# Kernel tuning notes

Measured on AMD Instinct MI355X. Metric: run time of the kernel, lower is better.

## Reference

```python
import jax, jax.numpy as jnp
import numpy as np

BN_EPS = 1e-5
NUM_BITS = 8          # activation quantization bits
NUM_BITS_WEIGHT = 8   # weight quantization bits


def _ste(x, q):
    # straight-through estimator: forward = q, backward = identity
    return x + jax.lax.stop_gradient(q - x)


def quant_signed(x, bits):
    # symmetric signed per-tensor uniform quantization (input_signed=True / weights with sign=True)
    qmax = float(2 ** (bits - 1) - 1)
    scale = jnp.max(jnp.abs(x)) / qmax + 1e-12
    q = jnp.clip(jnp.round(x / scale), -qmax - 1.0, qmax) * scale
    return _ste(x, q)


def quant_unsigned(x, bits):
    # unsigned per-tensor uniform quantization (input_signed=False, post-ReLU activations)
    qmax = float(2 ** bits - 1)
    scale = jnp.max(x) / qmax + 1e-12
    q = jnp.clip(jnp.round(x / scale), 0.0, qmax) * scale
    return _ste(x, q)


def conv3x3(x, w, stride=1):
    # x: [N,C,H,W], w: [O,I,3,3], padding=1, no bias
    return jax.lax.conv_general_dilated(
        x, w, window_strides=(stride, stride), padding=((1, 1), (1, 1)),
        dimension_numbers=('NCHW', 'OIHW', 'NCHW'))


def batchnorm(x, gamma, beta):
    # training-mode BN: per-batch statistics over (N,H,W)
    mean = jnp.mean(x, axis=(0, 2, 3), keepdims=True)
    var = jnp.var(x, axis=(0, 2, 3), keepdims=True)
    xn = (x - mean) * jax.lax.rsqrt(var + BN_EPS)
    return xn * gamma[None, :, None, None] + beta[None, :, None, None]


def setup_inputs() -> dict:
    key = jax.random.key(0)
    k1, k2, k3 = jax.random.split(key, 3)
    B, C, H, W = 64, 256, 32, 32
    x = jax.random.normal(k1, (B, C, H, W), dtype=jnp.float32)
    fan = C * 9
    w1 = jax.random.normal(k2, (C, C, 3, 3), dtype=jnp.float32) * np.sqrt(2.0 / fan)
    w2 = jax.random.normal(k3, (C, C, 3, 3), dtype=jnp.float32) * np.sqrt(2.0 / fan)
    gamma1 = jnp.ones((C,), jnp.float32)
    beta1 = jnp.zeros((C,), jnp.float32)
    gamma2 = jnp.ones((C,), jnp.float32)
    beta2 = jnp.zeros((C,), jnp.float32)
    return {'x': x, 'w1': w1, 'gamma1': gamma1, 'beta1': beta1,
            'w2': w2, 'gamma2': gamma2, 'beta2': beta2}


def reference(x, w1, gamma1, beta1, w2, gamma2, beta2):
    residual = x
    # conv1: input_signed=True -> signed 8-bit act quant; weight 8-bit signed quant
    qx = quant_signed(x, NUM_BITS)
    qw1 = quant_signed(w1, NUM_BITS_WEIGHT)
    out = conv3x3(qx, qw1, stride=1)
    out = batchnorm(out, gamma1, beta1)
    out = jax.nn.relu(out)
    # conv2: input_signed=False -> unsigned 8-bit act quant (post-ReLU)
    qo = quant_unsigned(out, NUM_BITS)
    qw2 = quant_signed(w2, NUM_BITS_WEIGHT)
    out = conv3x3(qo, qw2, stride=1)
    out = batchnorm(out, gamma2, beta2)
    out = out + residual
    out = jax.nn.relu(out)
    return out
```

## Files before the change

### kernel.cpp

```cpp
#include <hip/hip_runtime.h>

typedef __attribute__((ext_vector_type(4))) int i32x4;
typedef __attribute__((ext_vector_type(4))) float f32x4;

typedef __attribute__((address_space(1))) unsigned int uglobal;
typedef __attribute__((address_space(3))) unsigned int ulocal;

__device__ __forceinline__ void async16(const void* g, void* l) {
  __builtin_amdgcn_global_load_lds((const uglobal*)g, (ulocal*)l, 16, 0, 0);
}
__device__ __forceinline__ float u2f(unsigned u) { return __uint_as_float(u); }

__global__ __launch_bounds__(256) void absmax3_kernel(const float* __restrict__ x,
                                                      const float* __restrict__ w1,
                                                      const float* __restrict__ w2,
                                                      unsigned* __restrict__ sc) {
  int b = blockIdx.x;
  const float* src; int n4, b0, nb, seg;
  if (b < 1792)      { src = x;  n4 = 4194304; b0 = 0;    nb = 1792; seg = 0; }
  else if (b < 1856) { src = w1; n4 = 147456;  b0 = 1792; nb = 64;   seg = 1; }
  else               { src = w2; n4 = 147456;  b0 = 1856; nb = 64;   seg = 2; }
  float m = 0.f;
  int stride = nb * 256;
  for (int i = (b - b0) * 256 + threadIdx.x; i < n4; i += stride) {
    float4 v = ((const float4*)src)[i];
    m = fmaxf(fmaxf(fabsf(v.x), fabsf(v.y)), fmaxf(fmaxf(fabsf(v.z), fabsf(v.w)), m));
  }
  for (int off = 32; off; off >>= 1) m = fmaxf(m, __shfl_down(m, off, 64));
  __shared__ float sm[4];
  int lane = threadIdx.x & 63, wv = threadIdx.x >> 6;
  if (!lane) sm[wv] = m;
  __syncthreads();
  if (threadIdx.x == 0)
    atomicMax(sc + seg, __float_as_uint(fmaxf(fmaxf(sm[0], sm[1]), fmaxf(sm[2], sm[3]))));
}

__global__ __launch_bounds__(256) void quantw_kernel(const float* __restrict__ w1,
                                                     const float* __restrict__ w2,
                                                     signed char* __restrict__ wq1,
                                                     signed char* __restrict__ wq2,
                                                     const unsigned* __restrict__ sc) {
  int b = blockIdx.x;
  int t2 = b >= 2304;
  const float* w = t2 ? w2 : w1;
  signed char* wq = t2 ? wq2 : wq1;
  float s = u2f(sc[1 + t2]) / 127.f + 1e-12f;
  int j = (b - t2 * 2304) * 256 + threadIdx.x;
  int o = j / 2304, k = j - o * 2304, tap = k >> 8, c = k & 255;
  float q = fminf(fmaxf(rintf(w[(size_t)(o * 256 + c) * 9 + tap] / s), -128.f), 127.f);
  wq[j] = (signed char)q;
}

__global__ __launch_bounds__(64) void tapsum_kernel(const signed char* __restrict__ wq2,
                                                    int* __restrict__ csumT) {
  int o = blockIdx.x;
  const int* row = (const int*)(wq2 + (size_t)o * 2304);
  int s = 0;
  for (int i = threadIdx.x; i < 576; i += 64) {
    int v = row[i];
    s += (int)(signed char)(v) + (int)(signed char)(v >> 8) +
         (int)(signed char)(v >> 16) + (int)(signed char)(v >> 24);
  }
  for (int off = 32; off; off >>= 1) s += __shfl_down(s, off, 64);
  if (threadIdx.x == 0) csumT[o] = 128 * s;
}

__global__ __launch_bounds__(256) void quantx_kernel(const float* __restrict__ x,
                                                     signed char* __restrict__ halo,
                                                     const unsigned* __restrict__ sc) {
  int n = blockIdx.x >> 5, h = blockIdx.x & 31;
  float s = u2f(sc[0]) / 127.f + 1e-12f;
  __shared__ float lds[32 * 257];
  const float* src = x + (size_t)n * 262144 + h * 32;
  int t = threadIdx.x;
  int wloc = t & 31, crow = t >> 5;
  for (int cc = 0; cc < 256; cc += 8) {
    int c = cc + crow;
    lds[wloc * 257 + c] = src[(size_t)c * 1024 + wloc];
  }
  __syncthreads();
  signed char* dst = halo + ((size_t)((n * 34 + h + 1) * 34) + 1) * 256;
  int c4 = (t & 63) * 4, wsub = t >> 6;
  for (int j = 0; j < 8; ++j) {
    int w_ = wsub * 8 + j;
    char4 q;
    q.x = (signed char)fminf(fmaxf(rintf(lds[w_ * 257 + c4 + 0] / s), -128.f), 127.f);
    q.y = (signed char)fminf(fmaxf(rintf(lds[w_ * 257 + c4 + 1] / s), -128.f), 127.f);
    q.z = (signed char)fminf(fmaxf(rintf(lds[w_ * 257 + c4 + 2] / s), -128.f), 127.f);
    q.w = (signed char)fminf(fmaxf(rintf(lds[w_ * 257 + c4 + 3] / s), -128.f), 127.f);
    *(char4*)(dst + (size_t)w_ * 256 + c4) = q;
  }
}

template <int MODE>
__global__ __launch_bounds__(512) void conv_i8_kernel(const signed char* __restrict__ aptr,
                                                      const signed char* __restrict__ bptr,
                                                      float* __restrict__ out,
                                                      const unsigned* __restrict__ sc,
                                                      float* __restrict__ part,
                                                      const int* __restrict__ csumT) {
  extern __shared__ char smem[];
  const int tid = threadIdx.x, lane = tid & 63, wid = tid >> 6;
  const int wm = wid >> 2, wn = wid & 3;
  int bid = blockIdx.x;
  bid = (bid & 7) * 32 + (bid >> 3);
  const int pixBase = bid * 256;

  long gA[2], gB[2];
  int ldst[2];
#pragma unroll
  for (int j = 0; j < 2; ++j) {
    int d = tid * 16 + j * 8192;
    int rp = d >> 7, s5 = (d >> 4) & 7, sp = s5 ^ (rp & 7);
    int row = rp * 2 + (sp >> 2), kc = (sp & 3) * 16;
    ldst[j] = d;
    int p = pixBase + row;
    int n = p >> 10, h = (p >> 5) & 31, w_ = p & 31;
    long ghalo = (long)((n * 34 + h) * 34 + w_) * 256 + kc;
    long gwt = (long)row * 2304 + kc;
    gA[j] = (MODE == 0) ? ghalo : gwt;
    gB[j] = (MODE == 0) ? gwt : ghalo;
  }

  const int g = lane >> 4, l15 = lane & 15;
  int aOff[8], bOff[4];
#pragma unroll
  for (int m = 0; m < 8; ++m) {
    int row = wm * 128 + m * 16 + l15; int rp = row >> 1;
    aOff[m] = rp * 128 + (((((row & 1) << 2) | g) ^ (rp & 7)) << 4);
  }
#pragma unroll
  for (int n = 0; n < 4; ++n) {
    int row = wn * 64 + n * 16 + l15; int rp = row >> 1;
    bOff[n] = rp * 128 + (((((row & 1) << 2) | g) ^ (rp & 7)) << 4);
  }

  const char* ac = (const char*)aptr;
  const char* bc = (const char*)bptr;
  char* lds = smem;

  auto stage = [&](int P) {
    int cblk = P / 9, tap = P - cblk * 9;
    int kh = tap / 3, kw = tap - kh * 3;
    long uH = (long)(kh * 34 + kw) * 256 + cblk * 64;
    long uW = (long)tap * 256 + cblk * 64;
    long uA = (MODE == 0) ? uH : uW;
    long uB = (MODE == 0) ? uW : uH;
    char* rb = lds + (P & 3) * 32768;
    async16(ac + gA[0] + uA, rb + ldst[0]);
    async16(ac + gA[1] + uA, rb + ldst[1]);
    async16(bc + gB[0] + uB, rb + 16384 + ldst[0]);
    async16(bc + gB[1] + uB, rb + 16384 + ldst[1]);
  };

  i32x4 acc[8][4];
#pragma unroll
  for (int m = 0; m < 8; ++m)
#pragma unroll
    for (int n = 0; n < 4; ++n)
#pragma unroll
      for (int r = 0; r < 4; ++r) acc[m][n][r] = 0;

  stage(0); stage(1); stage(2);
  asm volatile("s_waitcnt vmcnt(8)" ::: "memory");
  asm volatile("s_barrier" ::: "memory");

  for (int P = 0; P < 36; ++P) {
    if (P < 33) stage(P + 3);
    const char* rb = lds + (P & 3) * 32768;
    i32x4 a[8], b[4];
#pragma unroll
    for (int m = 0; m < 8; ++m) a[m] = *(const i32x4*)(rb + aOff[m]);
#pragma unroll
    for (int n = 0; n < 4; ++n) b[n] = *(const i32x4*)(rb + 16384 + bOff[n]);
    __builtin_amdgcn_s_setprio(1);
#pragma unroll
    for (int m = 0; m < 8; ++m)
#pragma unroll
      for (int n = 0; n < 4; ++n)
        acc[m][n] = __builtin_amdgcn_mfma_i32_16x16x64_i8(a[m], b[n], acc[m][n], 0, 0, 0);
    __builtin_amdgcn_s_setprio(0);
    if (P < 33)       asm volatile("s_waitcnt vmcnt(8)" ::: "memory");
    else if (P == 33) asm volatile("s_waitcnt vmcnt(4)" ::: "memory");
    else if (P == 34) asm volatile("s_waitcnt vmcnt(0)" ::: "memory");
    if (P < 35) asm volatile("s_barrier" ::: "memory");
  }
  __syncthreads();

  float* twr = (float*)(smem + wid * 17408);

  if constexpr (MODE == 0) {
    const float s = (u2f(sc[0]) / 127.f + 1e-12f) * (u2f(sc[1]) / 127.f + 1e-12f);
    float vs[4], vss[4], vmx[4], vmn[4];
#pragma unroll
    for (int n = 0; n < 4; ++n) { vs[n] = 0.f; vss[n] = 0.f; vmx[n] = -3.4e38f; vmn[n] = 3.4e38f; }
#pragma unroll
    for (int half = 0; half < 2; ++half) {
#pragma unroll
      for (int m2 = 0; m2 < 4; ++m2) {
        int m = half * 4 + m2;
#pragma unroll
        for (int n = 0; n < 4; ++n)
#pragma unroll
          for (int r = 0; r < 4; ++r) {
            float v = (float)acc[m][n][r] * s;
            vs[n] += v; vss[n] += v * v;
            vmx[n] = fmaxf(vmx[n], v); vmn[n] = fminf(vmn[n], v);
            twr[(m2 * 16 + g * 4 + r) * 68 + n * 16 + l15] = v;
          }
      }
#pragma unroll
      for (int it = 0; it < 16; ++it) {
        int i = it * 64 + lane;
        int row = i >> 4, c4 = (i & 15) << 2;
        float4 v4 = *(const float4*)(twr + row * 68 + c4);
        int p = pixBase + wm * 128 + half * 64 + row;
        *(float4*)(out + (size_t)p * 256 + wn * 64 + c4) = v4;
      }
    }
#pragma unroll
    for (int off = 16; off <= 32; off <<= 1)
#pragma unroll
      for (int n = 0; n < 4; ++n) {
        vs[n] += __shfl_xor(vs[n], off, 64);
        vss[n] += __shfl_xor(vss[n], off, 64);
        vmx[n] = fmaxf(vmx[n], __shfl_xor(vmx[n], off, 64));
        vmn[n] = fminf(vmn[n], __shfl_xor(vmn[n], off, 64));
      }
    __syncthreads();
    float* S0 = (float*)(smem + 139264);
    float* S1 = S0 + 512; float* S2 = S0 + 1024; float* S3 = S0 + 1536;
    if (lane < 16) {
#pragma unroll
      for (int n = 0; n < 4; ++n) {
        int ch = wn * 64 + n * 16 + l15;
        S0[wm * 256 + ch] = vs[n]; S1[wm * 256 + ch] = vss[n];
        S2[wm * 256 + ch] = vmx[n]; S3[wm * 256 + ch] = vmn[n];
      }
    }
    __syncthreads();
    if (tid < 256) {
      int idx = bid * 256 + tid;
      part[idx]          = S0[tid] + S0[256 + tid];
      part[65536 + idx]  = S1[tid] + S1[256 + tid];
      part[131072 + idx] = fmaxf(S2[tid], S2[256 + tid]);
      part[196608 + idx] = fminf(S3[tid], S3[256 + tid]);
    }
  } else {
    const float s = (u2f(sc[3]) / 255.f + 1e-12f) * (u2f(sc[2]) / 127.f + 1e-12f);
    float* SS = (float*)(smem + 139264);
    float* SQ = SS + 1024;
#pragma unroll
    for (int half = 0; half < 2; ++half) {
#pragma unroll
      for (int m2 = 0; m2 < 4; ++m2) {
        int m = half * 4 + m2;
        int o0 = wm * 128 + half * 64 + m2 * 16 + g * 4;
        i32x4 tc = *(const i32x4*)(csumT + o0);
        float sr[4] = {0.f, 0.f, 0.f, 0.f}, sq[4] = {0.f, 0.f, 0.f, 0.f};
#pragma unroll
        for (int n = 0; n < 4; ++n)
#pragma unroll
          for (int r = 0; r < 4; ++r) {
            float v = (float)(acc[m][n][r] + tc[r]) * s;
            sr[r] += v; sq[r] += v * v;
            twr[(m2 * 16 + g * 4 + r) * 68 + n * 16 + l15] = v;
          }
#pragma unroll
        for (int off = 1; off <= 8; off <<= 1)
#pragma unroll
          for (int r = 0; r < 4; ++r) {
            sr[r] += __shfl_xor(sr[r], off, 64);
            sq[r] += __shfl_xor(sq[r], off, 64);
          }
        if (l15 == 0) {
#pragma unroll
          for (int r = 0; r < 4; ++r) {
            SS[wn * 256 + o0 + r] = sr[r];
            SQ[wn * 256 + o0 + r] = sq[r];
          }
        }
      }
#pragma unroll
      for (int it = 0; it < 16; ++it) {
        int i = it * 64 + lane;
        int row = i >> 4, c4 = (i & 15) << 2;
        float4 v4 = *(const float4*)(twr + row * 68 + c4);
        int o = wm * 128 + half * 64 + row;
        *(float4*)(out + (size_t)o * 65536 + pixBase + wn * 64 + c4) = v4;
      }
    }
    __syncthreads();
    if (tid < 256) {
      float a = 0.f, b = 0.f;
#pragma unroll
      for (int w = 0; w < 4; ++w) { a += SS[w * 256 + tid]; b += SQ[w * 256 + tid]; }
      part[bid * 256 + tid] = a;
      part[65536 + bid * 256 + tid] = b;
    }
  }
}

__global__ __launch_bounds__(256) void bn1fin_kernel(const float* __restrict__ part,
                                                     const float* __restrict__ g,
                                                     const float* __restrict__ be,
                                                     float* __restrict__ bnA, float* __restrict__ bnB,
                                                     unsigned* __restrict__ sc) {
  int o0 = blockIdx.x * 32;
  int t = threadIdx.x, oc = t & 31, mq = t >> 5;
  float s = 0.f, ss = 0.f, mx = -3.4e38f, mn = 3.4e38f;
  for (int j = 0; j < 32; ++j) {
    int i = (mq * 32 + j) * 256 + o0 + oc;
    s += part[i]; ss += part[65536 + i];
    mx = fmaxf(mx, part[131072 + i]); mn = fminf(mn, part[196608 + i]);
  }
  __shared__ float red[4][8][32];
  red[0][mq][oc] = s; red[1][mq][oc] = ss; red[2][mq][oc] = mx; red[3][mq][oc] = mn;
  __syncthreads();
  if (t < 32) {
    s = 0.f; ss = 0.f; mx = -3.4e38f; mn = 3.4e38f;
    for (int q = 0; q < 8; ++q) {
      s += red[0][q][t]; ss += red[1][q][t];
      mx = fmaxf(mx, red[2][q][t]); mn = fminf(mn, red[3][q][t]);
    }
    float mean = s * (1.f / 65536.f);
    float var = fmaxf(ss * (1.f / 65536.f) - mean * mean, 0.f);
    int o = o0 + t;
    float a = g[o] * rsqrtf(var + 1e-5f);
    float b2 = be[o] - mean * a;
    bnA[o] = a; bnB[o] = b2;
    float m = fmaxf(fmaxf(a * mx + b2, a * mn + b2), 0.f);
    atomicMax(sc + 3, __float_as_uint(m));
  }
}

__global__ __launch_bounds__(256) void bn2fin_kernel(const float* __restrict__ part,
                                                     const float* __restrict__ g,
                                                     const float* __restrict__ be,
                                                     float* __restrict__ bnA2, float* __restrict__ bnB2) {
  int o0 = blockIdx.x * 32;
  int t = threadIdx.x, oc = t & 31, mq = t >> 5;
  float s = 0.f, ss = 0.f;
  for (int j = 0; j < 32; ++j) {
    int i = (mq * 32 + j) * 256 + o0 + oc;
    s += part[i]; ss += part[65536 + i];
  }
  __shared__ float red[2][8][32];
  red[0][mq][oc] = s; red[1][mq][oc] = ss;
  __syncthreads();
  if (t < 32) {
    s = 0.f; ss = 0.f;
    for (int q = 0; q < 8; ++q) { s += red[0][q][t]; ss += red[1][q][t]; }
    float mean = s * (1.f / 65536.f);
    float var = fmaxf(ss * (1.f / 65536.f) - mean * mean, 0.f);
    int o = o0 + t;
    float a = g[o] * rsqrtf(var + 1e-5f);
    bnA2[o] = a;
    bnB2[o] = be[o] - mean * a;
  }
}

__global__ __launch_bounds__(256) void apply_kernel(const float* __restrict__ y,
                                                    const float* __restrict__ bnA,
                                                    const float* __restrict__ bnB,
                                                    const unsigned* __restrict__ sc,
                                                    signed char* __restrict__ halo) {
  int t = threadIdx.x;
  int c4 = (t & 63) * 4;
  int psub = t >> 6;
  float s2 = u2f(sc[3]) / 255.f + 1e-12f;
  float4 a = *(const float4*)(bnA + c4);
  float4 b = *(const float4*)(bnB + c4);
  int p0 = blockIdx.x * 16 + psub;
  for (int j = 0; j < 4; ++j) {
    int p = p0 + j * 4;
    float4 v = *(const float4*)(y + (size_t)p * 256 + c4);
    char4 q;
    q.x = (signed char)((int)fminf(fmaxf(rintf(fmaxf(a.x * v.x + b.x, 0.f) / s2), 0.f), 255.f) - 128);
    q.y = (signed char)((int)fminf(fmaxf(rintf(fmaxf(a.y * v.y + b.y, 0.f) / s2), 0.f), 255.f) - 128);
    q.z = (signed char)((int)fminf(fmaxf(rintf(fmaxf(a.z * v.z + b.z, 0.f) / s2), 0.f), 255.f) - 128);
    q.w = (signed char)((int)fminf(fmaxf(rintf(fmaxf(a.w * v.w + b.w, 0.f) / s2), 0.f), 255.f) - 128);
    int n = p >> 10, h = (p >> 5) & 31, w_ = p & 31;
    *(char4*)(halo + ((size_t)((n * 34 + h + 1) * 34) + (w_ + 1)) * 256 + c4) = q;
  }
}

__global__ __launch_bounds__(256) void final_kernel(const float* __restrict__ y2,
                                                    const float* __restrict__ x,
                                                    const float* __restrict__ bnA2,
                                                    const float* __restrict__ bnB2,
                                                    float* __restrict__ out) {
  int tid = blockIdx.x * 256 + threadIdx.x;
  for (int i = tid; i < 4194304; i += 1048576) {
    int e = i << 2;
    int o = (e >> 10) & 255;
    int n = e >> 18, hw = e & 1023;
    float4 v = *(const float4*)(y2 + (((size_t)o << 16) + (n << 10) + hw));
    float4 xr = ((const float4*)x)[i];
    float a = bnA2[o], b = bnB2[o];
    float4 r;
    r.x = fmaxf(a * v.x + b + xr.x, 0.f);
    r.y = fmaxf(a * v.y + b + xr.y, 0.f);
    r.z = fmaxf(a * v.z + b + xr.z, 0.f);
    r.w = fmaxf(a * v.w + b + xr.w, 0.f);
    ((float4*)out)[i] = r;
  }
}

extern "C" void kernel_launch(void* const* d_in, const int* in_sizes, int n_in,
                              void* d_out, int out_size, void* d_ws, size_t ws_size,
                              hipStream_t stream) {
  const float* x  = (const float*)d_in[0];
  const float* w1 = (const float*)d_in[1];
  const float* g1 = (const float*)d_in[2];
  const float* b1 = (const float*)d_in[3];
  const float* w2 = (const float*)d_in[4];
  const float* g2 = (const float*)d_in[5];
  const float* b2 = (const float*)d_in[6];
  float* out = (float*)d_out;
  char* ws = (char*)d_ws;

  unsigned* sc = (unsigned*)ws;
  float* bnA   = (float*)(ws + 4096);
  float* bnB   = (float*)(ws + 8192);
  float* bnA2  = (float*)(ws + 12288);
  float* bnB2  = (float*)(ws + 16384);
  int*   csumT = (int*)(ws + 20480);
  float* part  = (float*)(ws + 24576);
  signed char* wq1  = (signed char*)(ws + 24576 + 1048576);
  signed char* wq2  = wq1 + 589824;
  signed char* halo = wq2 + 589824;
  float* convb = (float*)(ws + 24576 + 1048576 + 2 * 589824 + 18939904);

  hipFuncSetAttribute((const void*)(conv_i8_kernel<0>), hipFuncAttributeMaxDynamicSharedMemorySize, 147456);
  hipFuncSetAttribute((const void*)(conv_i8_kernel<1>), hipFuncAttributeMaxDynamicSharedMemorySize, 147456);

  hipMemsetAsync(sc, 0, 64, stream);
  hipMemsetAsync(halo, 0, 18939904, stream);

  absmax3_kernel<<<1920, 256, 0, stream>>>(x, w1, w2, sc);
  quantw_kernel<<<4608, 256, 0, stream>>>(w1, w2, wq1, wq2, sc);
  tapsum_kernel<<<256, 64, 0, stream>>>(wq2, csumT);
  quantx_kernel<<<2048, 256, 0, stream>>>(x, halo, sc);
  conv_i8_kernel<0><<<256, 512, 147456, stream>>>(halo, wq1, convb, sc, part, csumT);
  bn1fin_kernel<<<8, 256, 0, stream>>>(part, g1, b1, bnA, bnB, sc);
  hipMemsetAsync(halo, 0x80, 18939904, stream);
  apply_kernel<<<4096, 256, 0, stream>>>(convb, bnA, bnB, sc, halo);
  conv_i8_kernel<1><<<256, 512, 147456, stream>>>(wq2, halo, convb, sc, part, csumT);
  bn2fin_kernel<<<8, 256, 0, stream>>>(part, g2, b2, bnA2, bnB2);
  final_kernel<<<4096, 256, 0, stream>>>(convb, x, bnA2, bnB2, out);
}
```

Measured before the change: 332.4 us.

## Split conv mainloop into half-stages, fuse weight quant with tapsum, fill only halo borders

The conv main loop is split into two halves. Each half reads its A fragments and issues half of the next stage's async loads before running its MFMAs, with extra barriers and sched_barriers to interleave LDS reads, global-to-LDS copies and matrix ops. Weight quantization is restructured to one block per output channel via LDS, writing quantized bytes coalesced and computing the conv2 tap sums in the same pass, which removes the separate tapsum kernel. The two full 19MB halo memsets are replaced by a small kernel that writes only the border cells, on the assumption that the interior is overwritten each time. The split adds barriers per iteration, which could stall the MFMA pipeline.

```diff
diff --git a/kernel.cpp b/kernel.cpp
--- a/kernel.cpp
+++ b/kernel.cpp
@@ -1,7 +1,6 @@
 #include <hip/hip_runtime.h>
 
 typedef __attribute__((ext_vector_type(4))) int i32x4;
-typedef __attribute__((ext_vector_type(4))) float f32x4;
 
 typedef __attribute__((address_space(1))) unsigned int uglobal;
 typedef __attribute__((address_space(3))) unsigned int ulocal;
@@ -39,30 +38,44 @@
                                                      const float* __restrict__ w2,
                                                      signed char* __restrict__ wq1,
                                                      signed char* __restrict__ wq2,
-                                                     const unsigned* __restrict__ sc) {
-  int b = blockIdx.x;
-  int t2 = b >= 2304;
-  const float* w = t2 ? w2 : w1;
-  signed char* wq = t2 ? wq2 : wq1;
-  float s = u2f(sc[1 + t2]) / 127.f + 1e-12f;
-  int j = (b - t2 * 2304) * 256 + threadIdx.x;
-  int o = j / 2304, k = j - o * 2304, tap = k >> 8, c = k & 255;
-  float q = fminf(fmaxf(rintf(w[(size_t)(o * 256 + c) * 9 + tap] / s), -128.f), 127.f);
-  wq[j] = (signed char)q;
-}
-
-__global__ __launch_bounds__(64) void tapsum_kernel(const signed char* __restrict__ wq2,
-                                                    int* __restrict__ csumT) {
-  int o = blockIdx.x;
-  const int* row = (const int*)(wq2 + (size_t)o * 2304);
-  int s = 0;
-  for (int i = threadIdx.x; i < 576; i += 64) {
-    int v = row[i];
-    s += (int)(signed char)(v) + (int)(signed char)(v >> 8) +
-         (int)(signed char)(v >> 16) + (int)(signed char)(v >> 24);
-  }
-  for (int off = 32; off; off >>= 1) s += __shfl_down(s, off, 64);
-  if (threadIdx.x == 0) csumT[o] = 128 * s;
+                                                     const unsigned* __restrict__ sc,
+                                                     int* __restrict__ csumT) {
+  int b = blockIdx.x, which = b >> 8, o = b & 255, t = threadIdx.x;
+  const float* w = which ? w2 : w1;
+  signed char* wq = which ? wq2 : wq1;
+  float s = u2f(sc[1 + which]) / 127.f + 1e-12f;
+  __shared__ float lw[2304];
+  for (int j = t; j < 2304; j += 256) lw[j] = w[(size_t)o * 2304 + j];
+  __syncthreads();
+  int ssum = 0;
+#pragma unroll
+  for (int tap = 0; tap < 9; ++tap) {
+    float q = fminf(fmaxf(rintf(lw[t * 9 + tap] / s), -128.f), 127.f);
+    wq[(size_t)o * 2304 + tap * 256 + t] = (signed char)q;
+    ssum += (int)q;
+  }
+  if (which) {
+    for (int off = 32; off; off >>= 1) ssum += __shfl_down(ssum, off, 64);
+    __shared__ int si[4];
+    if (!(t & 63)) si[t >> 6] = ssum;
+    __syncthreads();
+    if (t == 0) csumT[o] = 128 * (si[0] + si[1] + si[2] + si[3]);
+  }
+}
+
+__global__ __launch_bounds__(256) void border_kernel(signed char* __restrict__ halo, int v) {
+  int n = blockIdx.x;
+  int4 val = make_int4(v, v, v, v);
+  for (int it = 0; it < 9; ++it) {
+    int slot = it * 256 + threadIdx.x;
+    if (slot >= 2112) break;
+    int cell = slot >> 4, sub = slot & 15;
+    int h, w;
+    if (cell < 34)      { h = 0;  w = cell; }
+    else if (cell < 68) { h = 33; w = cell - 34; }
+    else { int j = cell - 68; h = 1 + (j >> 1); w = (j & 1) * 33; }
+    *(int4*)(halo + ((size_t)((n * 34 + h) * 34) + w) * 256 + sub * 16) = val;
+  }
 }
 
 __global__ __launch_bounds__(256) void quantx_kernel(const float* __restrict__ x,
@@ -139,18 +152,21 @@
   const char* bc = (const char*)bptr;
   char* lds = smem;
 
-  auto stage = [&](int P) {
+  auto stageH = [&](int P, int h) {
     int cblk = P / 9, tap = P - cblk * 9;
     int kh = tap / 3, kw = tap - kh * 3;
     long uH = (long)(kh * 34 + kw) * 256 + cblk * 64;
     long uW = (long)tap * 256 + cblk * 64;
-    long uA = (MODE == 0) ? uH : uW;
-    long uB = (MODE == 0) ? uW : uH;
     char* rb = lds + (P & 3) * 32768;
-    async16(ac + gA[0] + uA, rb + ldst[0]);
-    async16(ac + gA[1] + uA, rb + ldst[1]);
-    async16(bc + gB[0] + uB, rb + 16384 + ldst[0]);
-    async16(bc + gB[1] + uB, rb + 16384 + ldst[1]);
+    if (h == 0) {
+      long uA = (MODE == 0) ? uH : uW;
+      async16(ac + gA[0] + uA, rb + ldst[0]);
+      async16(ac + gA[1] + uA, rb + ldst[1]);
+    } else {
+      long uB = (MODE == 0) ? uW : uH;
+      async16(bc + gB[0] + uB, rb + 16384 + ldst[0]);
+      async16(bc + gB[1] + uB, rb + 16384 + ldst[1]);
+    }
   };
 
   i32x4 acc[8][4];
@@ -161,21 +177,38 @@
 #pragma unroll
       for (int r = 0; r < 4; ++r) acc[m][n][r] = 0;
 
-  stage(0); stage(1); stage(2);
+  stageH(0, 0); stageH(0, 1); stageH(1, 0); stageH(1, 1); stageH(2, 0); stageH(2, 1);
   asm volatile("s_waitcnt vmcnt(8)" ::: "memory");
-  asm volatile("s_barrier" ::: "memory");
+  __builtin_amdgcn_s_barrier();
 
   for (int P = 0; P < 36; ++P) {
-    if (P < 33) stage(P + 3);
     const char* rb = lds + (P & 3) * 32768;
     i32x4 a[8], b[4];
 #pragma unroll
-    for (int m = 0; m < 8; ++m) a[m] = *(const i32x4*)(rb + aOff[m]);
+    for (int m = 0; m < 4; ++m) a[m] = *(const i32x4*)(rb + aOff[m]);
 #pragma unroll
     for (int n = 0; n < 4; ++n) b[n] = *(const i32x4*)(rb + 16384 + bOff[n]);
+    if (P < 33) stageH(P + 3, 0);
+    __builtin_amdgcn_s_barrier();
+    asm volatile("s_waitcnt lgkmcnt(0)" ::: "memory");
+    __builtin_amdgcn_sched_barrier(0);
     __builtin_amdgcn_s_setprio(1);
 #pragma unroll
-    for (int m = 0; m < 8; ++m)
+    for (int m = 0; m < 4; ++m)
+#pragma unroll
+      for (int n = 0; n < 4; ++n)
+        acc[m][n] = __builtin_amdgcn_mfma_i32_16x16x64_i8(a[m], b[n], acc[m][n], 0, 0, 0);
+    __builtin_amdgcn_s_setprio(0);
+    __builtin_amdgcn_s_barrier();
+#pragma unroll
+    for (int m = 4; m < 8; ++m) a[m] = *(const i32x4*)(rb + aOff[m]);
+    if (P < 33) stageH(P + 3, 1);
+    __builtin_amdgcn_s_barrier();
+    asm volatile("s_waitcnt lgkmcnt(0)" ::: "memory");
+    __builtin_amdgcn_sched_barrier(0);
+    __builtin_amdgcn_s_setprio(1);
+#pragma unroll
+    for (int m = 4; m < 8; ++m)
 #pragma unroll
       for (int n = 0; n < 4; ++n)
         acc[m][n] = __builtin_amdgcn_mfma_i32_16x16x64_i8(a[m], b[n], acc[m][n], 0, 0, 0);
@@ -183,7 +216,7 @@
     if (P < 33)       asm volatile("s_waitcnt vmcnt(8)" ::: "memory");
     else if (P == 33) asm volatile("s_waitcnt vmcnt(4)" ::: "memory");
     else if (P == 34) asm volatile("s_waitcnt vmcnt(0)" ::: "memory");
-    if (P < 35) asm volatile("s_barrier" ::: "memory");
+    if (P < 35) __builtin_amdgcn_s_barrier();
   }
   __syncthreads();
 
@@ -436,15 +469,14 @@
   hipFuncSetAttribute((const void*)(conv_i8_kernel<1>), hipFuncAttributeMaxDynamicSharedMemorySize, 147456);
 
   hipMemsetAsync(sc, 0, 64, stream);
-  hipMemsetAsync(halo, 0, 18939904, stream);
+  border_kernel<<<64, 256, 0, stream>>>(halo, 0);
 
   absmax3_kernel<<<1920, 256, 0, stream>>>(x, w1, w2, sc);
-  quantw_kernel<<<4608, 256, 0, stream>>>(w1, w2, wq1, wq2, sc);
-  tapsum_kernel<<<256, 64, 0, stream>>>(wq2, csumT);
+  quantw_kernel<<<512, 256, 0, stream>>>(w1, w2, wq1, wq2, sc, csumT);
   quantx_kernel<<<2048, 256, 0, stream>>>(x, halo, sc);
   conv_i8_kernel<0><<<256, 512, 147456, stream>>>(halo, wq1, convb, sc, part, csumT);
   bn1fin_kernel<<<8, 256, 0, stream>>>(part, g1, b1, bnA, bnB, sc);
-  hipMemsetAsync(halo, 0x80, 18939904, stream);
+  border_kernel<<<64, 256, 0, stream>>>(halo, (int)0x80808080u);
   apply_kernel<<<4096, 256, 0, stream>>>(convb, bnA, bnB, sc, halo);
   conv_i8_kernel<1><<<256, 512, 147456, stream>>>(wq2, halo, convb, sc, part, csumT);
   bn2fin_kernel<<<8, 256, 0, stream>>>(part, g2, b2, bnA2, bnB2);
```

Result: faster. 315.8 us (-5.0%).
